# Kernel tuning notes

Hardware: AMD Instinct MI355X
Metric: run time of the kernel (lower is better)

The kernel has to match this reference:

```python
import jax, jax.numpy as jnp
import numpy as np
from math import sqrt

# dims
B, H, P, N, D = 4, 8, 32, 32, 16   # batch, heads, n_patches, channels, patch_len
L = P * N                           # 1024 token positions
SEQ, PRED, WIN, E, NF = 512, 96, 10, 2, 6  # seq_len, pred_len, attention_window, e_layers, n_fore
EPS = float(np.finfo(np.float32).eps)      # torch RMSNorm default eps (finfo eps)


def setup_inputs() -> dict:
    key = jax.random.key(0)
    ks = jax.random.split(key, 8)
    return dict(
        tokens=jax.random.normal(ks[0], (B, H, L, D), jnp.float32),
        x_original=jax.random.normal(ks[1], (B, SEQ, N), jnp.float32),
        log_scales=jnp.full((E,), np.log(2.0), jnp.float32),
        attn_norm_w=jnp.ones((E, D), jnp.float32),
        conv_up_w=jax.random.normal(ks[2], (E, 2 * H, 1, 3), jnp.float32) * 0.1,
        conv_down_w=jax.random.normal(ks[3], (E, H, 2, 1), jnp.float32) * 0.1,
        ffn_norm_w=jnp.ones((E, D), jnp.float32),
        mix_w=jax.random.normal(ks[4], (1, H), jnp.float32) * 0.3,
        mix_b=jnp.zeros((1,), jnp.float32),
        fore_w=jax.random.normal(ks[5], (NF, P), jnp.float32) * 0.1,
        fore_b=jnp.zeros((NF,), jnp.float32),
    )


def _rms(x, w):
    # torch.nn.RMSNorm over last dim (patch_len)
    return x * jax.lax.rsqrt(jnp.mean(x * x, axis=-1, keepdims=True) + EPS) * w


def _mask():
    # pid repeated per-channel; True entries are masked out
    pid = jnp.repeat(jnp.arange(P), N)
    diff = pid[None, :] - pid[:, None]  # pid[key] - pid[query]
    return (diff <= 0) | (diff >= WIN)  # [L, L]


def _signed_attn(h, log_scale, mask):
    # scores: [B,H,L,L]; A = softmax(+s) - softmax(-s) with banded mask
    scores = jnp.einsum('bhld,bhmd->bhlm', h, h)
    scale = jnp.clip(jnp.exp(log_scale), 1.0, 30.0) / sqrt(D)
    pos = jnp.where(mask, -10000.0, scores)
    neg = jnp.where(mask, -10000.0, -scores)
    A = jax.nn.softmax(scale * pos, axis=-1) - jax.nn.softmax(scale * neg, axis=-1)
    return jnp.einsum('bhlm,bhmd->bhld', A, h)


def _conv_ffn(x, up_w, down_w, norm_w):
    # depthwise causal conv along patch time dim D; x: [B,H,L,D]
    r = x.transpose(0, 2, 1, 3).reshape(B * L, H, D)
    r = jnp.pad(r, ((0, 0), (0, 0), (2, 0)))  # causal left-pad (kernel_size-1)
    dn = ('NCH', 'OIH', 'NCH')
    r = jax.lax.conv_general_dilated(r, up_w, (1,), 'VALID', dimension_numbers=dn, feature_group_count=H)
    r = jax.nn.gelu(r, approximate=False)
    r = jax.lax.conv_general_dilated(r, down_w, (1,), 'VALID', dimension_numbers=dn, feature_group_count=H)
    r = r.reshape(B, L, H, D).transpose(0, 2, 1, 3)
    return _rms(x + r, norm_w)


def reference(tokens, x_original, log_scales, attn_norm_w, conv_up_w, conv_down_w,
              ffn_norm_w, mix_w, mix_b, fore_w, fore_b):
    mask = _mask()
    h = tokens
    for l in range(E):
        h = _rms(h + _signed_attn(h, log_scales[l], mask), attn_norm_w[l])
        h = _conv_ffn(h, conv_up_w[l], conv_down_w[l], ffn_norm_w[l])
    # aggregate heads -> forecast
    h = h.reshape(B, H, P, N, D).transpose(0, 3, 4, 2, 1)       # (B,N,D,P,H)
    h = jnp.einsum('bndph,h->bndp', h, mix_w[0]) + mix_b[0]      # channel_mixing
    f = jnp.einsum('bndp,fp->bndf', h, fore_w) + fore_b          # fore_projection
    f = f.reshape(B, N, D * NF)[:, :, -PRED:]                    # flatten + tail slice
    forecast = f.transpose(0, 2, 1)                              # (B,pred_len,N)
    return forecast, x_original
```

## Files before the change

kernel.cpp:

```cpp
#include <hip/hip_runtime.h>
#include <hip/hip_bf16.h>
#include <math.h>

#define BB 4
#define HH 8
#define PP 32
#define NN 32
#define DD 16
#define LL 1024
#define WINW 10
#define NFF 6
#define PREDL 96
#define SEQL 512
#define EPSF 1.1920928955078125e-07f
#define KROW 24
#define KTS 296
#define PROW 40
#define XROW 20

typedef __attribute__((ext_vector_type(8))) short bf16x8;
typedef __attribute__((ext_vector_type(4))) float f32x4;

__device__ inline short f2bs(float f) {
    __hip_bfloat16 h = __float2bfloat16(f);
    return *reinterpret_cast<short*>(&h);
}

__global__ __launch_bounds__(256) void layer_kernel(
    const float* __restrict__ hin, float* __restrict__ hout,
    const float* __restrict__ log_scales, const float* __restrict__ attn_norm,
    const float* __restrict__ up_w, const float* __restrict__ down_w,
    const float* __restrict__ ffn_norm, int layer,
    const float* __restrict__ xsrc, float* __restrict__ xdst)
{
    __shared__ short hK[9 * 32 * KROW];
    __shared__ short VT[16 * KTS];
    __shared__ short Pp[4][16 * PROW];
    __shared__ short Pn[4][16 * PROW];
    __shared__ float xls[32 * XROW];
    __shared__ float comb[2][64][8];
    __shared__ float combl[2][2][16];

    int blk = blockIdx.x;
    int bh  = blk >> 5;
    int hh  = bh & 7;
    int p0  = blk & 31;
    int nstage = min(9, (PP - 1) - p0);

    int tid  = threadIdx.x;
    int wid  = tid >> 6;
    int qh   = wid >> 1;
    int ch   = wid & 1;
    int lane = tid & 63;
    int quad = lane >> 4, n16 = lane & 15;

    if (xsrc && tid < 16) {
        const float4* x4 = (const float4*)xsrc;
        float4* o4 = (float4*)xdst;
        o4[blk * 16 + tid] = x4[blk * 16 + tid];
    }

    {
        const float4* src = (const float4*)(hin + ((size_t)bh * LL + (p0 + 1) * NN) * DD);
        int nf4 = nstage * 128;
        #pragma unroll
        for (int k = 0; k < 5; ++k) {
            int i = tid + k * 256;
            if (i < nf4) {
                int row = i >> 2, j = i & 3;
                float4 v = src[i];
                short s0 = f2bs(v.x), s1 = f2bs(v.y), s2 = f2bs(v.z), s3 = f2bs(v.w);
                unsigned long long u =
                      (unsigned long long)(unsigned short)s0
                    | ((unsigned long long)(unsigned short)s1 << 16)
                    | ((unsigned long long)(unsigned short)s2 << 32)
                    | ((unsigned long long)(unsigned short)s3 << 48);
                *(unsigned long long*)&hK[row * KROW + j * 4] = u;
                int d0 = j * 4;
                VT[(d0 + 0) * KTS + row] = s0;
                VT[(d0 + 1) * KTS + row] = s1;
                VT[(d0 + 2) * KTS + row] = s2;
                VT[(d0 + 3) * KTS + row] = s3;
            }
        }
    }

    bf16x8 Aq;
    #pragma unroll
    for (int j = 0; j < 8; ++j) Aq[j] = 0;
    if (quad < 2) {
        const float* qp = hin + ((size_t)bh * LL + p0 * NN + qh * 16 + n16) * DD + quad * 8;
        #pragma unroll
        for (int j = 0; j < 8; ++j) Aq[j] = f2bs(qp[j]);
    }
    float rs[4] = {0.f, 0.f, 0.f, 0.f};
    if (ch == 0) {
        #pragma unroll
        for (int r = 0; r < 4; ++r)
            rs[r] = hin[((size_t)bh * LL + p0 * NN + qh * 16 + quad * 4 + r) * DD + n16];
    }

    float sc  = fminf(fmaxf(__expf(log_scales[layer]), 1.0f), 30.0f) * 0.25f;
    float sc2 = sc * 1.4426950408889634f;

    __syncthreads();

    f32x4 Op, On;
    Op[0] = Op[1] = Op[2] = Op[3] = 0.f;
    On[0] = On[1] = On[2] = On[3] = 0.f;
    float lpp[4] = {0.f, 0.f, 0.f, 0.f}, lnn[4] = {0.f, 0.f, 0.f, 0.f};
    short* myPp = Pp[wid];
    short* myPn = Pn[wid];

    int c0 = ch ? 4 : 0;
    int c1 = ch ? nstage : min(4, nstage);

    for (int c = c0; c < c1; ++c) {
        int kb = c * 32;
        #pragma unroll
        for (int kt = 0; kt < 2; ++kt) {
            bf16x8 Bk;
            #pragma unroll
            for (int j = 0; j < 8; ++j) Bk[j] = 0;
            if (quad < 2)
                Bk = *(const bf16x8*)&hK[(kb + kt * 16 + n16) * KROW + quad * 8];
            f32x4 z; z[0] = z[1] = z[2] = z[3] = 0.f;
            f32x4 S = __builtin_amdgcn_mfma_f32_16x16x32_bf16(Aq, Bk, z, 0, 0, 0);
            #pragma unroll
            for (int r = 0; r < 4; ++r) {
                float t  = sc2 * S[r];
                float ep = exp2f(t);
                float en = exp2f(-t);
                lpp[r] += ep; lnn[r] += en;
                int pr = quad * 4 + r, pc = kt * 16 + n16;
                myPp[pr * PROW + pc] = f2bs(ep);
                myPn[pr * PROW + pc] = f2bs(en);
            }
        }
        bf16x8 Bv = *(const bf16x8*)&VT[n16 * KTS + kb + quad * 8];
        bf16x8 Ap = *(const bf16x8*)&myPp[n16 * PROW + quad * 8];
        bf16x8 An = *(const bf16x8*)&myPn[n16 * PROW + quad * 8];
        Op = __builtin_amdgcn_mfma_f32_16x16x32_bf16(Ap, Bv, Op, 0, 0, 0);
        On = __builtin_amdgcn_mfma_f32_16x16x32_bf16(An, Bv, On, 0, 0, 0);
    }

    #pragma unroll
    for (int r = 0; r < 4; ++r) {
        float a = lpp[r], b = lnn[r];
        a += __shfl_xor(a, 1); a += __shfl_xor(a, 2); a += __shfl_xor(a, 4); a += __shfl_xor(a, 8);
        b += __shfl_xor(b, 1); b += __shfl_xor(b, 2); b += __shfl_xor(b, 4); b += __shfl_xor(b, 8);
        lpp[r] = a; lnn[r] = b;
    }

    if (ch == 1) {
        *(f32x4*)&comb[qh][lane][0] = Op;
        *(f32x4*)&comb[qh][lane][4] = On;
        if (n16 == 0) {
            #pragma unroll
            for (int r = 0; r < 4; ++r) {
                combl[qh][0][quad * 4 + r] = lpp[r];
                combl[qh][1][quad * 4 + r] = lnn[r];
            }
        }
    }
    __syncthreads();
    if (ch == 1) return;

    {
        f32x4 o2 = *(const f32x4*)&comb[qh][lane][0];
        f32x4 n2 = *(const f32x4*)&comb[qh][lane][4];
        #pragma unroll
        for (int r = 0; r < 4; ++r) {
            Op[r] += o2[r];
            On[r] += n2[r];
            lpp[r] += combl[qh][0][quad * 4 + r];
            lnn[r] += combl[qh][1][quad * 4 + r];
        }
    }

    #pragma unroll
    for (int r = 0; r < 4; ++r) {
        float lp = lpp[r], ln = lnn[r];
        float rl = (lp > 0.f) ? (1.0f / lp) : 0.f;
        float rn = (ln > 0.f) ? (1.0f / ln) : 0.f;
        float v  = rs[r] + Op[r] * rl - On[r] * rn;
        float ss = v * v;
        ss += __shfl_xor(ss, 1); ss += __shfl_xor(ss, 2);
        ss += __shfl_xor(ss, 4); ss += __shfl_xor(ss, 8);
        float rr = rsqrtf(ss * (1.0f / 16.0f) + EPSF);
        xls[(qh * 16 + quad * 4 + r) * XROW + n16] = v * rr * attn_norm[layer * DD + n16];
    }

    {
        int q = qh * 16 + n16;
        int g = quad;

        const float* uw = up_w + (size_t)(layer * 2 * HH + 2 * hh) * 3;
        float w00 = uw[0], w01 = uw[1], w02 = uw[2];
        float w10 = uw[3], w11 = uw[4], w12 = uw[5];
        const float* dw = down_w + (size_t)(layer * HH + hh) * 2;
        float dc0 = dw[0], dc1 = dw[1];

        float xm2 = g ? xls[q * XROW + 4 * g - 2] : 0.f;
        float xm1 = g ? xls[q * XROW + 4 * g - 1] : 0.f;
        float4 xv = *(const float4*)&xls[q * XROW + 4 * g];
        float xa[6] = {xm2, xm1, xv.x, xv.y, xv.z, xv.w};

        float v4[4], ss = 0.f;
        #pragma unroll
        for (int i = 0; i < 4; ++i) {
            float u0 = w00 * xa[i] + w01 * xa[i + 1] + w02 * xa[i + 2];
            float u1 = w10 * xa[i] + w11 * xa[i + 1] + w12 * xa[i + 2];
            float g0 = 0.5f * u0 * (1.0f + erff(u0 * 0.7071067811865475f));
            float g1 = 0.5f * u1 * (1.0f + erff(u1 * 0.7071067811865475f));
            float vv = xa[i + 2] + dc0 * g0 + dc1 * g1;
            v4[i] = vv; ss += vv * vv;
        }
        ss += __shfl_xor(ss, 16); ss += __shfl_xor(ss, 32);
        float r2 = rsqrtf(ss * (1.0f / 16.0f) + EPSF);

        const float4 fn = *(const float4*)&ffn_norm[layer * DD + 4 * g];
        float* op = hout + ((size_t)bh * LL + p0 * NN + q) * DD + 4 * g;
        float4 o;
        o.x = v4[0] * r2 * fn.x;
        o.y = v4[1] * r2 * fn.y;
        o.z = v4[2] * r2 * fn.z;
        o.w = v4[3] * r2 * fn.w;
        *(float4*)op = o;
    }
}

__global__ __launch_bounds__(256) void tail_kernel(
    const float* __restrict__ h, const float* __restrict__ mw_,
    const float* __restrict__ mb_, const float* __restrict__ fw_,
    const float* __restrict__ fb_, float* __restrict__ out)
{
    int b   = blockIdx.x;
    int tid = threadIdx.x;
    int n   = tid >> 3;
    int d0  = (2 * tid) & 15;

    float mw[8];
    #pragma unroll
    for (int k = 0; k < 8; ++k) mw[k] = mw_[k];
    float mb = mb_[0];

    float acc0[NFF] = {0.f, 0.f, 0.f, 0.f, 0.f, 0.f};
    float acc1[NFF] = {0.f, 0.f, 0.f, 0.f, 0.f, 0.f};

    for (int p = 0; p < PP; ++p) {
        float m0 = mb, m1 = mb;
        #pragma unroll
        for (int k = 0; k < 8; ++k) {
            const float* hp = h + (size_t)(((b * HH + k) * LL) + p * NN + n) * DD + d0;
            float2 hv = *(const float2*)hp;
            m0 += hv.x * mw[k];
            m1 += hv.y * mw[k];
        }
        #pragma unroll
        for (int fi = 0; fi < NFF; ++fi) {
            float w = fw_[fi * PP + p];
            acc0[fi] += m0 * w;
            acc1[fi] += m1 * w;
        }
    }
    #pragma unroll
    for (int fi = 0; fi < NFF; ++fi) {
        float fb = fb_[fi];
        out[((b * DD + d0) * NFF + fi) * NN + n]     = acc0[fi] + fb;
        out[((b * DD + d0 + 1) * NFF + fi) * NN + n] = acc1[fi] + fb;
    }
}

static int find_by_size(const int* s, int n, int want, int occurrence) {
    int seen = 0;
    for (int i = 0; i < n; ++i)
        if (s[i] == want) { if (seen == occurrence) return i; ++seen; }
    return -1;
}

extern "C" void kernel_launch(void* const* d_in, const int* in_sizes, int n_in,
                              void* d_out, int out_size, void* d_ws, size_t ws_size,
                              hipStream_t stream) {
    int it  = find_by_size(in_sizes, n_in, 524288, 0);
    int ix  = find_by_size(in_sizes, n_in, 65536, 0);
    int ils = find_by_size(in_sizes, n_in, 2, 0);
    int ian = find_by_size(in_sizes, n_in, 32, 0);
    int icu = find_by_size(in_sizes, n_in, 96, 0);
    int icd = find_by_size(in_sizes, n_in, 32, 1);
    int ifn = find_by_size(in_sizes, n_in, 32, 2);
    int imw = find_by_size(in_sizes, n_in, 8, 0);
    int imb = find_by_size(in_sizes, n_in, 1, 0);
    int ifw = find_by_size(in_sizes, n_in, 192, 0);
    int ifb = find_by_size(in_sizes, n_in, 6, 0);
    if (it < 0 || ix < 0 || ils < 0 || ian < 0 || icu < 0 || icd < 0 ||
        ifn < 0 || imw < 0 || imb < 0 || ifw < 0 || ifb < 0) {
        it = 0; ix = 1; ils = 2; ian = 3; icu = 4; icd = 5; ifn = 6;
        imw = 7; imb = 8; ifw = 9; ifb = 10;
    }

    const float* tokens     = (const float*)d_in[it];
    const float* x_orig     = (const float*)d_in[ix];
    const float* log_scales = (const float*)d_in[ils];
    const float* attn_norm  = (const float*)d_in[ian];
    const float* up_w       = (const float*)d_in[icu];
    const float* down_w     = (const float*)d_in[icd];
    const float* ffn_norm   = (const float*)d_in[ifn];
    const float* mix_w      = (const float*)d_in[imw];
    const float* mix_b      = (const float*)d_in[imb];
    const float* fore_w     = (const float*)d_in[ifw];
    const float* fore_b     = (const float*)d_in[ifb];
    float* out = (float*)d_out;

    const size_t NH = (size_t)BB * HH * LL * DD;
    float* hA = (float*)d_ws;
    float* hB = hA + NH;

    layer_kernel<<<1024, 256, 0, stream>>>(tokens, hA, log_scales, attn_norm,
                                           up_w, down_w, ffn_norm, 0,
                                           x_orig, out + BB * PREDL * NN);
    layer_kernel<<<1024, 256, 0, stream>>>(hA, hB, log_scales, attn_norm,
                                           up_w, down_w, ffn_norm, 1,
                                           (const float*)nullptr, (float*)nullptr);
    tail_kernel<<<BB, 256, 0, stream>>>(hB, mix_w, mix_b, fore_w, fore_b, out);
}
```

Measured before the change: 118.6 us.

## Fuse both layers and tail into one persistent kernel with grid barriers

Merges the two layer launches and the forecast tail into a single kernel, separated by atomic-counter grid barriers, with a memset to reset the counters. This removes the inter-kernel launch gaps. All 1024 blocks must be co-resident, and a non-cooperative launch does not guarantee that, so the barrier could deadlock. Spinning also adds some cost.

```diff
diff --git a/kernel.cpp b/kernel.cpp
--- a/kernel.cpp
+++ b/kernel.cpp
@@ -17,6 +17,7 @@
 #define KTS 296
 #define PROW 40
 #define XROW 20
+#define NBLK 1024
 
 typedef __attribute__((ext_vector_type(8))) short bf16x8;
 typedef __attribute__((ext_vector_type(4))) float f32x4;
@@ -26,39 +27,35 @@
     return *reinterpret_cast<short*>(&h);
 }
 
-__global__ __launch_bounds__(256) void layer_kernel(
+__device__ __forceinline__ void grid_barrier_wait(unsigned* bar) {
+    __syncthreads();
+    if (threadIdx.x == 0) {
+        __threadfence();
+        __hip_atomic_fetch_add(bar, 1u, __ATOMIC_ACQ_REL, __HIP_MEMORY_SCOPE_AGENT);
+        while (__hip_atomic_load(bar, __ATOMIC_ACQUIRE, __HIP_MEMORY_SCOPE_AGENT) < NBLK) {}
+        __threadfence();
+    }
+    __syncthreads();
+}
+
+__device__ __forceinline__ void layer_body(
     const float* __restrict__ hin, float* __restrict__ hout,
     const float* __restrict__ log_scales, const float* __restrict__ attn_norm,
     const float* __restrict__ up_w, const float* __restrict__ down_w,
-    const float* __restrict__ ffn_norm, int layer,
-    const float* __restrict__ xsrc, float* __restrict__ xdst)
+    const float* __restrict__ ffn_norm, int layer, int blk, int tid,
+    short* hK, short* VT, short (*Pp)[16 * PROW], short (*Pn)[16 * PROW],
+    float* xls, float (*comb)[64][8], float (*combl)[2][16])
 {
-    __shared__ short hK[9 * 32 * KROW];
-    __shared__ short VT[16 * KTS];
-    __shared__ short Pp[4][16 * PROW];
-    __shared__ short Pn[4][16 * PROW];
-    __shared__ float xls[32 * XROW];
-    __shared__ float comb[2][64][8];
-    __shared__ float combl[2][2][16];
-
-    int blk = blockIdx.x;
     int bh  = blk >> 5;
     int hh  = bh & 7;
     int p0  = blk & 31;
     int nstage = min(9, (PP - 1) - p0);
 
-    int tid  = threadIdx.x;
     int wid  = tid >> 6;
     int qh   = wid >> 1;
     int ch   = wid & 1;
     int lane = tid & 63;
     int quad = lane >> 4, n16 = lane & 15;
-
-    if (xsrc && tid < 16) {
-        const float4* x4 = (const float4*)xsrc;
-        float4* o4 = (float4*)xdst;
-        o4[blk * 16 + tid] = x4[blk * 16 + tid];
-    }
 
     {
         const float4* src = (const float4*)(hin + ((size_t)bh * LL + (p0 + 1) * NN) * DD);
@@ -164,111 +161,153 @@
         }
     }
     __syncthreads();
-    if (ch == 1) return;
+
+    if (ch == 0) {
+        {
+            f32x4 o2 = *(const f32x4*)&comb[qh][lane][0];
+            f32x4 n2 = *(const f32x4*)&comb[qh][lane][4];
+            #pragma unroll
+            for (int r = 0; r < 4; ++r) {
+                Op[r] += o2[r];
+                On[r] += n2[r];
+                lpp[r] += combl[qh][0][quad * 4 + r];
+                lnn[r] += combl[qh][1][quad * 4 + r];
+            }
+        }
+
+        #pragma unroll
+        for (int r = 0; r < 4; ++r) {
+            float lp = lpp[r], ln = lnn[r];
+            float rl = (lp > 0.f) ? (1.0f / lp) : 0.f;
+            float rn = (ln > 0.f) ? (1.0f / ln) : 0.f;
+            float v  = rs[r] + Op[r] * rl - On[r] * rn;
+            float ss = v * v;
+            ss += __shfl_xor(ss, 1); ss += __shfl_xor(ss, 2);
+            ss += __shfl_xor(ss, 4); ss += __shfl_xor(ss, 8);
+            float rr = rsqrtf(ss * (1.0f / 16.0f) + EPSF);
+            xls[(qh * 16 + quad * 4 + r) * XROW + n16] = v * rr * attn_norm[layer * DD + n16];
+        }
+
+        {
+            int q = qh * 16 + n16;
+            int g = quad;
+
+            const float* uw = up_w + (size_t)(layer * 2 * HH + 2 * hh) * 3;
+            float w00 = uw[0], w01 = uw[1], w02 = uw[2];
+            float w10 = uw[3], w11 = uw[4], w12 = uw[5];
+            const float* dw = down_w + (size_t)(layer * HH + hh) * 2;
+            float dc0 = dw[0], dc1 = dw[1];
+
+            float xm2 = g ? xls[q * XROW + 4 * g - 2] : 0.f;
+            float xm1 = g ? xls[q * XROW + 4 * g - 1] : 0.f;
+            float4 xv = *(const float4*)&xls[q * XROW + 4 * g];
+            float xa[6] = {xm2, xm1, xv.x, xv.y, xv.z, xv.w};
+
+            float v4[4], ss = 0.f;
+            #pragma unroll
+            for (int i = 0; i < 4; ++i) {
+                float u0 = w00 * xa[i] + w01 * xa[i + 1] + w02 * xa[i + 2];
+                float u1 = w10 * xa[i] + w11 * xa[i + 1] + w12 * xa[i + 2];
+                float g0 = 0.5f * u0 * (1.0f + erff(u0 * 0.7071067811865475f));
+                float g1 = 0.5f * u1 * (1.0f + erff(u1 * 0.7071067811865475f));
+                float vv = xa[i + 2] + dc0 * g0 + dc1 * g1;
+                v4[i] = vv; ss += vv * vv;
+            }
+            ss += __shfl_xor(ss, 16); ss += __shfl_xor(ss, 32);
+            float r2 = rsqrtf(ss * (1.0f / 16.0f) + EPSF);
+
+            const float4 fn = *(const float4*)&ffn_norm[layer * DD + 4 * g];
+            float* op = hout + ((size_t)bh * LL + p0 * NN + q) * DD + 4 * g;
+            float4 o;
+            o.x = v4[0] * r2 * fn.x;
+            o.y = v4[1] * r2 * fn.y;
+            o.z = v4[2] * r2 * fn.z;
+            o.w = v4[3] * r2 * fn.w;
+            *(float4*)op = o;
+        }
+    }
+}
+
+__global__ __launch_bounds__(256) void fused_kernel(
+    const float* __restrict__ tokens, float* __restrict__ hA, float* __restrict__ hB,
+    float* __restrict__ out,
+    const float* __restrict__ log_scales, const float* __restrict__ attn_norm,
+    const float* __restrict__ up_w, const float* __restrict__ down_w,
+    const float* __restrict__ ffn_norm,
+    const float* __restrict__ mix_w, const float* __restrict__ mix_b,
+    const float* __restrict__ fore_w, const float* __restrict__ fore_b,
+    const float* __restrict__ x_orig, unsigned* __restrict__ bars)
+{
+    __shared__ short hK[9 * 32 * KROW];
+    __shared__ short VT[16 * KTS];
+    __shared__ short Pp[4][16 * PROW];
+    __shared__ short Pn[4][16 * PROW];
+    __shared__ float xls[32 * XROW];
+    __shared__ float comb[2][64][8];
+    __shared__ float combl[2][2][16];
+
+    int blk = blockIdx.x;
+    int tid = threadIdx.x;
+
+    if (tid < 16) {
+        const float4* x4 = (const float4*)x_orig;
+        float4* o4 = (float4*)(out + BB * PREDL * NN);
+        o4[blk * 16 + tid] = x4[blk * 16 + tid];
+    }
+
+    layer_body(tokens, hA, log_scales, attn_norm, up_w, down_w, ffn_norm, 0,
+               blk, tid, hK, VT, Pp, Pn, xls, comb, combl);
+    grid_barrier_wait(&bars[0]);
+    layer_body(hA, hB, log_scales, attn_norm, up_w, down_w, ffn_norm, 1,
+               blk, tid, hK, VT, Pp, Pn, xls, comb, combl);
+
+    __syncthreads();
+    if (tid == 0) {
+        __threadfence();
+        __hip_atomic_fetch_add(&bars[1], 1u, __ATOMIC_ACQ_REL, __HIP_MEMORY_SCOPE_AGENT);
+    }
+    if (blk >= BB) return;
+    if (tid == 0) {
+        while (__hip_atomic_load(&bars[1], __ATOMIC_ACQUIRE, __HIP_MEMORY_SCOPE_AGENT) < NBLK) {}
+        __threadfence();
+    }
+    __syncthreads();
 
     {
-        f32x4 o2 = *(const f32x4*)&comb[qh][lane][0];
-        f32x4 n2 = *(const f32x4*)&comb[qh][lane][4];
-        #pragma unroll
-        for (int r = 0; r < 4; ++r) {
-            Op[r] += o2[r];
-            On[r] += n2[r];
-            lpp[r] += combl[qh][0][quad * 4 + r];
-            lnn[r] += combl[qh][1][quad * 4 + r];
-        }
-    }
-
-    #pragma unroll
-    for (int r = 0; r < 4; ++r) {
-        float lp = lpp[r], ln = lnn[r];
-        float rl = (lp > 0.f) ? (1.0f / lp) : 0.f;
-        float rn = (ln > 0.f) ? (1.0f / ln) : 0.f;
-        float v  = rs[r] + Op[r] * rl - On[r] * rn;
-        float ss = v * v;
-        ss += __shfl_xor(ss, 1); ss += __shfl_xor(ss, 2);
-        ss += __shfl_xor(ss, 4); ss += __shfl_xor(ss, 8);
-        float rr = rsqrtf(ss * (1.0f / 16.0f) + EPSF);
-        xls[(qh * 16 + quad * 4 + r) * XROW + n16] = v * rr * attn_norm[layer * DD + n16];
-    }
-
-    {
-        int q = qh * 16 + n16;
-        int g = quad;
-
-        const float* uw = up_w + (size_t)(layer * 2 * HH + 2 * hh) * 3;
-        float w00 = uw[0], w01 = uw[1], w02 = uw[2];
-        float w10 = uw[3], w11 = uw[4], w12 = uw[5];
-        const float* dw = down_w + (size_t)(layer * HH + hh) * 2;
-        float dc0 = dw[0], dc1 = dw[1];
-
-        float xm2 = g ? xls[q * XROW + 4 * g - 2] : 0.f;
-        float xm1 = g ? xls[q * XROW + 4 * g - 1] : 0.f;
-        float4 xv = *(const float4*)&xls[q * XROW + 4 * g];
-        float xa[6] = {xm2, xm1, xv.x, xv.y, xv.z, xv.w};
-
-        float v4[4], ss = 0.f;
-        #pragma unroll
-        for (int i = 0; i < 4; ++i) {
-            float u0 = w00 * xa[i] + w01 * xa[i + 1] + w02 * xa[i + 2];
-            float u1 = w10 * xa[i] + w11 * xa[i + 1] + w12 * xa[i + 2];
-            float g0 = 0.5f * u0 * (1.0f + erff(u0 * 0.7071067811865475f));
-            float g1 = 0.5f * u1 * (1.0f + erff(u1 * 0.7071067811865475f));
-            float vv = xa[i + 2] + dc0 * g0 + dc1 * g1;
-            v4[i] = vv; ss += vv * vv;
-        }
-        ss += __shfl_xor(ss, 16); ss += __shfl_xor(ss, 32);
-        float r2 = rsqrtf(ss * (1.0f / 16.0f) + EPSF);
-
-        const float4 fn = *(const float4*)&ffn_norm[layer * DD + 4 * g];
-        float* op = hout + ((size_t)bh * LL + p0 * NN + q) * DD + 4 * g;
-        float4 o;
-        o.x = v4[0] * r2 * fn.x;
-        o.y = v4[1] * r2 * fn.y;
-        o.z = v4[2] * r2 * fn.z;
-        o.w = v4[3] * r2 * fn.w;
-        *(float4*)op = o;
-    }
-}
-
-__global__ __launch_bounds__(256) void tail_kernel(
-    const float* __restrict__ h, const float* __restrict__ mw_,
-    const float* __restrict__ mb_, const float* __restrict__ fw_,
-    const float* __restrict__ fb_, float* __restrict__ out)
-{
-    int b   = blockIdx.x;
-    int tid = threadIdx.x;
-    int n   = tid >> 3;
-    int d0  = (2 * tid) & 15;
-
-    float mw[8];
-    #pragma unroll
-    for (int k = 0; k < 8; ++k) mw[k] = mw_[k];
-    float mb = mb_[0];
-
-    float acc0[NFF] = {0.f, 0.f, 0.f, 0.f, 0.f, 0.f};
-    float acc1[NFF] = {0.f, 0.f, 0.f, 0.f, 0.f, 0.f};
-
-    for (int p = 0; p < PP; ++p) {
-        float m0 = mb, m1 = mb;
-        #pragma unroll
-        for (int k = 0; k < 8; ++k) {
-            const float* hp = h + (size_t)(((b * HH + k) * LL) + p * NN + n) * DD + d0;
-            float2 hv = *(const float2*)hp;
-            m0 += hv.x * mw[k];
-            m1 += hv.y * mw[k];
+        int b   = blk;
+        int n   = tid >> 3;
+        int d0  = (2 * tid) & 15;
+
+        float mw[8];
+        #pragma unroll
+        for (int k = 0; k < 8; ++k) mw[k] = mix_w[k];
+        float mb = mix_b[0];
+
+        float acc0[NFF] = {0.f, 0.f, 0.f, 0.f, 0.f, 0.f};
+        float acc1[NFF] = {0.f, 0.f, 0.f, 0.f, 0.f, 0.f};
+
+        for (int p = 0; p < PP; ++p) {
+            float m0 = mb, m1 = mb;
+            #pragma unroll
+            for (int k = 0; k < 8; ++k) {
+                const float* hp = hB + (size_t)(((b * HH + k) * LL) + p * NN + n) * DD + d0;
+                float2 hv = *(const float2*)hp;
+                m0 += hv.x * mw[k];
+                m1 += hv.y * mw[k];
+            }
+            #pragma unroll
+            for (int fi = 0; fi < NFF; ++fi) {
+                float w = fore_w[fi * PP + p];
+                acc0[fi] += m0 * w;
+                acc1[fi] += m1 * w;
+            }
         }
         #pragma unroll
         for (int fi = 0; fi < NFF; ++fi) {
-            float w = fw_[fi * PP + p];
-            acc0[fi] += m0 * w;
-            acc1[fi] += m1 * w;
-        }
-    }
-    #pragma unroll
-    for (int fi = 0; fi < NFF; ++fi) {
-        float fb = fb_[fi];
-        out[((b * DD + d0) * NFF + fi) * NN + n]     = acc0[fi] + fb;
-        out[((b * DD + d0 + 1) * NFF + fi) * NN + n] = acc1[fi] + fb;
+            float fb = fore_b[fi];
+            out[((b * DD + d0) * NFF + fi) * NN + n]     = acc0[fi] + fb;
+            out[((b * DD + d0 + 1) * NFF + fi) * NN + n] = acc1[fi] + fb;
+        }
     }
 }
 
@@ -315,12 +354,15 @@
     const size_t NH = (size_t)BB * HH * LL * DD;
     float* hA = (float*)d_ws;
     float* hB = hA + NH;
-
-    layer_kernel<<<1024, 256, 0, stream>>>(tokens, hA, log_scales, attn_norm,
-                                           up_w, down_w, ffn_norm, 0,
-                                           x_orig, out + BB * PREDL * NN);
-    layer_kernel<<<1024, 256, 0, stream>>>(hA, hB, log_scales, attn_norm,
-                                           up_w, down_w, ffn_norm, 1,
-                                           (const float*)nullptr, (float*)nullptr);
-    tail_kernel<<<BB, 256, 0, stream>>>(hB, mix_w, mix_b, fore_w, fore_b, out);
-}
+    unsigned* bars = (unsigned*)(hB + NH);
+
+    hipMemsetAsync(bars, 0, 64, stream);
+
+    void* args[] = {
+        (void*)&tokens, (void*)&hA, (void*)&hB, (void*)&out,
+        (void*)&log_scales, (void*)&attn_norm, (void*)&up_w, (void*)&down_w,
+        (void*)&ffn_norm, (void*)&mix_w, (void*)&mix_b, (void*)&fore_w,
+        (void*)&fore_b, (void*)&x_orig, (void*)&bars
+    };
+    hipLaunchKernel((void*)fused_kernel, dim3(NBLK), dim3(256), args, 0, stream);
+}
```

Result: slower. 266.1 us (+124.3%).
